# Kernel optimization log

Hardware: AMD Instinct MI355X
Metric: run time of the kernel (lower is better)

## Reference

```python
import jax, jax.numpy as jnp
import numpy as np

MARGIN = 1.0
SAFE_RADIUS = 4.0
B, C, H, W = 16, 48, 64, 64
N_CORR = 2048


def _normalize(x, eps=1e-12):
    # F.normalize(x, dim=0): L2-normalize over the channel axis
    return x / jnp.maximum(jnp.linalg.norm(x, axis=0, keepdims=True), eps)


def _grid_positions(h, w):
    i, j = jnp.meshgrid(jnp.arange(h, dtype=jnp.float32),
                        jnp.arange(w, dtype=jnp.float32), indexing='ij')
    return jnp.stack([i.reshape(-1), j.reshape(-1)], axis=0)


def _per_image(df1, df2, att1, att2, ids, fp2):
    c, h1, w1 = df1.shape
    _, h2, w2 = df2.shape
    all_d1 = _normalize(df1.reshape(c, -1))   # [c, h1*w1]
    all_d2 = _normalize(df2.reshape(c, -1))   # [c, h2*w2]

    d1 = all_d1[:, ids]                       # [c, n] gathered anchors
    s1 = att1.reshape(-1)[ids]                # [n]
    d2 = _normalize(df2[:, fp2[0], fp2[1]])   # [c, n] gathered positives

    positive_distance = 2.0 - 2.0 * jnp.sum(d1 * d2, axis=0)  # [n]

    # hard-negative mining in image 2
    grid2 = _grid_positions(h2, w2)           # [2, h2*w2]
    pd2 = jnp.max(jnp.abs(fp2.astype(jnp.float32)[:, :, None] - grid2[:, None, :]), axis=0)
    out2 = (pd2 > SAFE_RADIUS).astype(df1.dtype)            # [n, h2*w2]
    dm2 = 2.0 - 2.0 * jnp.einsum('cn,cm->nm', d1, all_d2)   # [n, h2*w2]
    neg2 = jnp.min(dm2 + (1.0 - out2) * 10.0, axis=1)       # [n]

    # hard-negative mining in image 1
    grid1 = _grid_positions(h1, w1)
    fp1 = grid1[:, ids]                                      # [2, n]
    pd1 = jnp.max(jnp.abs(fp1[:, :, None] - grid1[:, None, :]), axis=0)
    out1 = (pd1 > SAFE_RADIUS).astype(df1.dtype)
    dm1 = 2.0 - 2.0 * jnp.einsum('cn,cm->nm', d2, all_d1)
    neg1 = jnp.min(dm1 + (1.0 - out1) * 10.0, axis=1)

    diff = positive_distance - jnp.minimum(neg1, neg2)
    s2 = att2[0, fp2[0], fp2[1]]
    w = s1 * s2
    return jnp.sum(w * jax.nn.relu(MARGIN + diff)) / jnp.sum(w)


def setup_inputs() -> dict:
    key = jax.random.key(0)
    k1, k2, k3, k4, k5, k6 = jax.random.split(key, 6)
    return {
        'x1_encoded': jax.random.normal(k1, (B, C, H, W), dtype=jnp.float32),
        'x2_encoded': jax.random.normal(k2, (B, C, H, W), dtype=jnp.float32),
        'attentions1': jax.random.uniform(k3, (B, 1, H, W), dtype=jnp.float32),
        'attentions2': jax.random.uniform(k4, (B, 1, H, W), dtype=jnp.float32),
        'ids': jax.random.randint(k5, (B, N_CORR), 0, H * W),
        'fmap_pos2': jax.random.randint(k6, (B, 2, N_CORR), 0, H),
    }


def reference(x1_encoded, x2_encoded, attentions1, attentions2, ids, fmap_pos2):
    per_image = jax.vmap(_per_image)(x1_encoded, x2_encoded, attentions1,
                                     attentions2, ids, fmap_pos2)
    return jnp.mean(per_image).reshape(1)
```

## Files before the change

### kernel.cpp

```cpp
#include <hip/hip_runtime.h>
#include <stdint.h>

#define BB 16
#define HW 4096
#define NC 2048
#define KHW 72
#define KB 144

typedef __attribute__((ext_vector_type(8))) __bf16 bf16x8;
typedef __attribute__((ext_vector_type(8))) short short8;
typedef __attribute__((ext_vector_type(4))) float floatx4;

static __device__ __forceinline__ unsigned short f2bf(float f) {
    unsigned u = __builtin_bit_cast(unsigned, f);
    unsigned r = u + 0x7fffu + ((u >> 16) & 1u);
    return (unsigned short)(r >> 16);
}

#define GLD16(g, l) __builtin_amdgcn_global_load_lds((const __attribute__((address_space(1))) void*)(g), (__attribute__((address_space(3))) void*)(l), 16, 0, 0)
#define GLD4(g, l)  __builtin_amdgcn_global_load_lds((const __attribute__((address_space(1))) void*)(g), (__attribute__((address_space(3))) void*)(l), 4, 0, 0)

__global__ void prep_fused(const float* __restrict__ x1, const float* __restrict__ x2,
                           const int* __restrict__ ids, const int* __restrict__ fp2,
                           unsigned short* __restrict__ dbp,
                           int* __restrict__ perm, int* __restrict__ qcol_s,
                           int* __restrict__ aqpack, unsigned int* __restrict__ maxs2enc) {
    __shared__ __align__(16) unsigned char slab[36864];
    int bid = blockIdx.x, tid = threadIdx.x;
    if (bid < 512) {
        int img = bid >> 8;
        int b = (bid & 255) >> 4;
        int p0 = (bid & 15) * 256;
        int p = p0 + tid;
        const float* x = img ? x2 : x1;
        const float* col = x + (size_t)b * 48 * HW + p;
        float v[48]; float s = 0.f;
#pragma unroll
        for (int c = 0; c < 48; ++c) { v[c] = col[c * HW]; s = fmaf(v[c], v[c], s); }
        float r = 1.f / fmaxf(sqrtf(s), 1e-12f);
        unsigned short* lcol = (unsigned short*)(slab + tid * KB);
#pragma unroll
        for (int ch = 0; ch < 6; ++ch) {
            union { unsigned u[4]; floatx4 f; } pk;
#pragma unroll
            for (int d = 0; d < 4; ++d) {
                int c = ch * 8 + d * 2;
                pk.u[d] = (unsigned)f2bf(v[c] * r) | ((unsigned)f2bf(v[c + 1] * r) << 16);
            }
            *(floatx4*)(lcol + ch * 8) = pk.f;
        }
        floatx4 z = {0.f, 0.f, 0.f, 0.f};
#pragma unroll
        for (int ch = 6; ch < 9; ++ch) *(floatx4*)(lcol + ch * 8) = z;
        __syncthreads();
        unsigned char* dstb = (unsigned char*)dbp + ((size_t)(img * BB + b) * HW + p0) * KB;
#pragma unroll
        for (int rr = 0; rr < 9; ++rr) {
            int idx = rr * 4096 + tid * 16;
            *(floatx4*)(dstb + idx) = *(const floatx4*)(slab + idx);
        }
    } else if (bid < 544) {
        int* hist = (int*)slab;
        int* base = hist + 64;
        int seg = bid - 512;
        int dir = seg >> 4, b = seg & 15;
        if (tid < 64) hist[tid] = 0;
        __syncthreads();
#pragma unroll
        for (int k = 0; k < 8; ++k) {
            int n = k * 256 + tid;
            int idv = ids[b * NC + n];
            int i2 = fp2[b * 2 * NC + n];
            int qi = (dir == 0) ? i2 : (idv >> 6);
            atomicAdd(&hist[qi], 1);
        }
        __syncthreads();
        if (tid == 0) {
            int run = 0;
            for (int k = 0; k < 64; ++k) { base[k] = run; run += hist[k]; }
        }
        __syncthreads();
#pragma unroll
        for (int k = 0; k < 8; ++k) {
            int n = k * 256 + tid;
            int idv = ids[b * NC + n];
            int i2 = fp2[b * 2 * NC + n];
            int j2 = fp2[b * 2 * NC + NC + n];
            int qi, qj, qcol;
            if (dir == 0) { qi = i2; qj = j2; qcol = idv; }
            else          { qi = idv >> 6; qj = idv & 63; qcol = i2 * 64 + j2; }
            int slot = atomicAdd(&base[qi], 1);
            perm[seg * NC + slot] = n;
            qcol_s[seg * NC + slot] = qcol;
            aqpack[seg * NC + slot] = (qi << 8) | qj;
        }
    } else {
        int t = (bid - 544) * 256 + tid;
        uint4* p = (uint4*)maxs2enc;
        uint4 z = {0u, 0u, 0u, 0u};
#pragma unroll
        for (int k = 0; k < 8; ++k) p[k * 2048 + t] = z;
    }
}

static __device__ __forceinline__ void dma64(const unsigned char* g, unsigned char* l,
                                             int wave, int lane) {
    int wo = wave * 2304;
#pragma unroll
    for (int rr = 0; rr < 2; ++rr)
        GLD16(g + wo + rr * 1024 + lane * 16, l + wo + rr * 1024);
    GLD4(g + wo + 2048 + lane * 4, l + wo + 2048);
}

__global__ __launch_bounds__(256) void maxscore_mfma(
    const unsigned short* __restrict__ dbp,
    const int* __restrict__ perm, const int* __restrict__ qcol_s,
    const int* __restrict__ aqpack, unsigned int* __restrict__ maxs2enc) {
    __shared__ __align__(16) unsigned char smem[18432];

    int tid = threadIdx.x, wave = tid >> 6, lane = tid & 63;
    int quad = lane >> 4, cl = lane & 15;
    int gid = blockIdx.x;
    int seg = gid & 31, dir = seg >> 4, b = seg & 15;
    int rest = gid >> 5, mtile = rest & 7, nq = rest >> 3;
    int qbase = mtile * 256;
    int dbimg = 1 - dir;

    const unsigned char* dbQ = (const unsigned char*)(dbp + (size_t)(dir * BB + b) * HW * KHW);
    short8 afr[4][2];
#pragma unroll
    for (int t = 0; t < 4; ++t) {
        int slot = qbase + wave * 64 + t * 16 + cl;
        int qc = qcol_s[seg * NC + slot];
        const unsigned char* src = dbQ + (size_t)qc * KB;
        afr[t][0] = *(const short8*)(src + quad * 16);
        afr[t][1] = *(const short8*)(src + 64 + quad * 16);
    }
    int aqp2[4][2];
#pragma unroll
    for (int t = 0; t < 4; ++t)
#pragma unroll
        for (int pp = 0; pp < 2; ++pp) {
            int s0 = seg * NC + qbase + wave * 64 + t * 16 + quad * 4 + pp * 2;
            aqp2[t][pp] = aqpack[s0] | (aqpack[s0 + 1] << 16);
        }
    int wb = seg * NC + qbase + wave * 64;
    int qimin = __builtin_amdgcn_readfirstlane(aqpack[wb] >> 8);
    int qimax = __builtin_amdgcn_readfirstlane(aqpack[wb + 63] >> 8);

    const unsigned char* dsrc =
        (const unsigned char*)(dbp + ((size_t)(dbimg * BB + b) * HW + nq * 512) * KHW);
    dma64(dsrc, smem, wave, lane);

    const floatx4 zf = {0.f, 0.f, 0.f, 0.f};
    float cl_f = (float)cl;
    float mx[4][4];
#pragma unroll
    for (int t = 0; t < 4; ++t)
#pragma unroll
        for (int r = 0; r < 4; ++r) mx[t][r] = -1e30f;

    for (int tile = 0; tile < 8; ++tile) {
        unsigned char* buf = smem + (tile & 1) * 9216;
        __syncthreads();
        if (tile + 1 < 8)
            dma64(dsrc + (tile + 1) * 9216, smem + ((tile + 1) & 1) * 9216, wave, lane);
        int mi = nq * 8 + tile;
        bool active = (mi >= qimin - 4) && (mi <= qimax + 4);
        if (active) {
            float mi_f = (float)mi;
            float qjd[4][4];
#pragma unroll
            for (int t = 0; t < 4; ++t)
#pragma unroll
                for (int r = 0; r < 4; ++r) {
                    int ap = (aqp2[t][r >> 1] >> (16 * (r & 1))) & 0xffff;
                    bool rowblk = fabsf((float)(ap >> 8) - mi_f) <= 4.0f;
                    qjd[t][r] = rowblk ? ((float)(ap & 255) - cl_f) : 1e6f;
                }
#pragma unroll
            for (int js = 0; js < 4; ++js) {
                float jj = (float)(js * 16);
                short8 b0 = *(const short8*)(buf + (js * 16 + cl) * KB + quad * 16);
                short8 b1 = *(const short8*)(buf + (js * 16 + cl) * KB + 64 + quad * 16);
#pragma unroll
                for (int t = 0; t < 4; ++t) {
                    floatx4 acc = __builtin_amdgcn_mfma_f32_16x16x32_bf16(
                        __builtin_bit_cast(bf16x8, afr[t][0]),
                        __builtin_bit_cast(bf16x8, b0), zf, 0, 0, 0);
                    acc = __builtin_amdgcn_mfma_f32_16x16x32_bf16(
                        __builtin_bit_cast(bf16x8, afr[t][1]),
                        __builtin_bit_cast(bf16x8, b1), acc, 0, 0, 0);
#pragma unroll
                    for (int r = 0; r < 4; ++r) {
                        bool ok = fabsf(qjd[t][r] - jj) > 4.0f;
                        mx[t][r] = ok ? fmaxf(mx[t][r], acc[r]) : mx[t][r];
                    }
                }
            }
        } else {
#pragma unroll
            for (int js = 0; js < 4; ++js) {
                short8 b0 = *(const short8*)(buf + (js * 16 + cl) * KB + quad * 16);
                short8 b1 = *(const short8*)(buf + (js * 16 + cl) * KB + 64 + quad * 16);
#pragma unroll
                for (int t = 0; t < 4; ++t) {
                    floatx4 acc = __builtin_amdgcn_mfma_f32_16x16x32_bf16(
                        __builtin_bit_cast(bf16x8, afr[t][0]),
                        __builtin_bit_cast(bf16x8, b0), zf, 0, 0, 0);
                    acc = __builtin_amdgcn_mfma_f32_16x16x32_bf16(
                        __builtin_bit_cast(bf16x8, afr[t][1]),
                        __builtin_bit_cast(bf16x8, b1), acc, 0, 0, 0);
#pragma unroll
                    for (int r = 0; r < 4; ++r)
                        mx[t][r] = fmaxf(mx[t][r], acc[r]);
                }
            }
        }
    }

#pragma unroll
    for (int t = 0; t < 4; ++t)
#pragma unroll
        for (int r = 0; r < 4; ++r) {
            float v = mx[t][r];
            v = fmaxf(v, __shfl_xor(v, 1, 16));
            v = fmaxf(v, __shfl_xor(v, 2, 16));
            v = fmaxf(v, __shfl_xor(v, 4, 16));
            v = fmaxf(v, __shfl_xor(v, 8, 16));
            mx[t][r] = v;
        }
    if (cl == 0) {
#pragma unroll
        for (int t = 0; t < 4; ++t)
#pragma unroll
            for (int r = 0; r < 4; ++r) {
                int slot = qbase + wave * 64 + t * 16 + quad * 4 + r;
                int orig = perm[seg * NC + slot];
                float v = mx[t][r] + 2.0f;
                atomicMax(&maxs2enc[(size_t)seg * NC + orig],
                          __builtin_bit_cast(unsigned, v));
            }
    }
}

__global__ void loss_kernel(const float* __restrict__ att1, const float* __restrict__ att2,
                            const int* __restrict__ ids, const int* __restrict__ fp2,
                            const unsigned short* __restrict__ dbp,
                            const unsigned int* __restrict__ maxs2enc,
                            float* __restrict__ pnum, float* __restrict__ pden) {
    int b = blockIdx.x >> 3, chunk = blockIdx.x & 7;
    int tid = threadIdx.x;
    int n = chunk * 256 + tid;
    int idv = ids[b * NC + n];
    int i2 = fp2[b * 2 * NC + n], j2 = fp2[b * 2 * NC + NC + n];
    const uint4* a4 = (const uint4*)(dbp + ((size_t)(0 * BB + b) * HW + idv) * KHW);
    const uint4* b4 = (const uint4*)(dbp + ((size_t)(1 * BB + b) * HW + i2 * 64 + j2) * KHW);
    float dot = 0.f;
#pragma unroll
    for (int i = 0; i < 6; ++i) {
        uint4 xa = a4[i], xb = b4[i];
        const unsigned* xu = (const unsigned*)&xa;
        const unsigned* yu = (const unsigned*)&xb;
#pragma unroll
        for (int w = 0; w < 4; ++w) {
            float xl = __builtin_bit_cast(float, xu[w] << 16);
            float xh = __builtin_bit_cast(float, xu[w] & 0xffff0000u);
            float yl = __builtin_bit_cast(float, yu[w] << 16);
            float yh = __builtin_bit_cast(float, yu[w] & 0xffff0000u);
            dot = fmaf(xl, yl, fmaf(xh, yh, dot));
        }
    }
    float m0 = __builtin_bit_cast(float, maxs2enc[(size_t)(0 * BB + b) * NC + n]) - 2.0f;
    float m1 = __builtin_bit_cast(float, maxs2enc[(size_t)(1 * BB + b) * NC + n]) - 2.0f;
    float ms = fmaxf(m0, m1);
    float diff = (2.f - 2.f * dot) - (2.f - 2.f * ms);
    float w = att1[b * HW + idv] * att2[b * HW + i2 * 64 + j2];
    float num = w * fmaxf(0.f, 1.f + diff);
    float den = w;
    __shared__ float sn[256], sd[256];
    sn[tid] = num; sd[tid] = den;
    __syncthreads();
    for (int s = 128; s > 0; s >>= 1) {
        if (tid < s) { sn[tid] += sn[tid + s]; sd[tid] += sd[tid + s]; }
        __syncthreads();
    }
    if (tid == 0) { pnum[blockIdx.x] = sn[0]; pden[blockIdx.x] = sd[0]; }
}

__global__ void final_kernel(const float* __restrict__ pnum, const float* __restrict__ pden,
                             float* __restrict__ out) {
    int tid = threadIdx.x;
    __shared__ float r[16];
    if (tid < 16) {
        float n = 0.f, d = 0.f;
#pragma unroll
        for (int c = 0; c < 8; ++c) { n += pnum[tid * 8 + c]; d += pden[tid * 8 + c]; }
        r[tid] = n / d;
    }
    __syncthreads();
    if (tid == 0) {
        float s = 0.f;
#pragma unroll
        for (int k = 0; k < 16; ++k) s += r[k];
        out[0] = s * (1.f / BB);
    }
}

extern "C" void kernel_launch(void* const* d_in, const int* in_sizes, int n_in,
                              void* d_out, int out_size, void* d_ws, size_t ws_size,
                              hipStream_t stream) {
    const float* x1  = (const float*)d_in[0];
    const float* x2  = (const float*)d_in[1];
    const float* att1 = (const float*)d_in[2];
    const float* att2 = (const float*)d_in[3];
    const int* ids   = (const int*)d_in[4];
    const int* fp2   = (const int*)d_in[5];
    float* out = (float*)d_out;

    unsigned char* w = (unsigned char*)d_ws;
    unsigned short* dbp = (unsigned short*)(w + 0);
    int* perm    = (int*)(w + 18874368);
    int* qcol_s  = (int*)(w + 19136512);
    int* aqpack  = (int*)(w + 19398656);
    unsigned int* maxs2enc = (unsigned int*)(w + 19660800);
    float* pnum  = (float*)(w + 19922944);
    float* pden  = (float*)(w + 19923456);

    prep_fused<<<dim3(552), dim3(256), 0, stream>>>(x1, x2, ids, fp2, dbp,
                                                    perm, qcol_s, aqpack, maxs2enc);
    maxscore_mfma<<<dim3(2048), dim3(256), 0, stream>>>(dbp, perm, qcol_s, aqpack, maxs2enc);
    loss_kernel<<<dim3(128), dim3(256), 0, stream>>>(att1, att2, ids, fp2, dbp, maxs2enc, pnum, pden);
    final_kernel<<<dim3(1), dim3(64), 0, stream>>>(pnum, pden, out);
}
```

Baseline: 144.5 us.

## Switch max-score kernel to 32x32x16 MFMA with tighter bf16 row padding

The similarity-max kernel moves from 16x16x32 MFMA tiles in 256-thread blocks to single-wave 64-thread blocks using 32x32x16 MFMA. Each block now covers 64 queries and 1024 database columns, double-buffered through LDS with 16-byte global-to-LDS loads. The packed bf16 descriptor row is cut from 144 to 112 bytes (48 channels plus padding), which shrinks both the prep writes and the per-tile DMA. The prep kernel now reads channels with float4 loads per wave and reduces the norms through LDS. The costs are a larger accumulator register footprint and more, smaller blocks, and the loss kernel must read the new 56-element row stride correctly.

After: 174.8 us. 21.0% more time.

```diff
diff --git a/kernel.cpp b/kernel.cpp
--- a/kernel.cpp
+++ b/kernel.cpp
@@ -4,12 +4,13 @@
 #define BB 16
 #define HW 4096
 #define NC 2048
-#define KHW 72
-#define KB 144
+#define KHW 56
+#define KB 112
 
 typedef __attribute__((ext_vector_type(8))) __bf16 bf16x8;
 typedef __attribute__((ext_vector_type(8))) short short8;
 typedef __attribute__((ext_vector_type(4))) float floatx4;
+typedef __attribute__((ext_vector_type(16))) float floatx16;
 
 static __device__ __forceinline__ unsigned short f2bf(float f) {
     unsigned u = __builtin_bit_cast(unsigned, f);
@@ -18,44 +19,54 @@
 }
 
 #define GLD16(g, l) __builtin_amdgcn_global_load_lds((const __attribute__((address_space(1))) void*)(g), (__attribute__((address_space(3))) void*)(l), 16, 0, 0)
-#define GLD4(g, l)  __builtin_amdgcn_global_load_lds((const __attribute__((address_space(1))) void*)(g), (__attribute__((address_space(3))) void*)(l), 4, 0, 0)
 
 __global__ void prep_fused(const float* __restrict__ x1, const float* __restrict__ x2,
                            const int* __restrict__ ids, const int* __restrict__ fp2,
                            unsigned short* __restrict__ dbp,
                            int* __restrict__ perm, int* __restrict__ qcol_s,
                            int* __restrict__ aqpack, unsigned int* __restrict__ maxs2enc) {
-    __shared__ __align__(16) unsigned char slab[36864];
+    __shared__ __align__(16) unsigned char slab[33792];
     int bid = blockIdx.x, tid = threadIdx.x;
     if (bid < 512) {
         int img = bid >> 8;
-        int b = (bid & 255) >> 4;
+        int b = (bid >> 4) & 15;
         int p0 = (bid & 15) * 256;
-        int p = p0 + tid;
+        int w = tid >> 6, l = tid & 63;
         const float* x = img ? x2 : x1;
-        const float* col = x + (size_t)b * 48 * HW + p;
-        float v[48]; float s = 0.f;
-#pragma unroll
-        for (int c = 0; c < 48; ++c) { v[c] = col[c * HW]; s = fmaf(v[c], v[c], s); }
-        float r = 1.f / fmaxf(sqrtf(s), 1e-12f);
-        unsigned short* lcol = (unsigned short*)(slab + tid * KB);
-#pragma unroll
-        for (int ch = 0; ch < 6; ++ch) {
-            union { unsigned u[4]; floatx4 f; } pk;
-#pragma unroll
-            for (int d = 0; d < 4; ++d) {
-                int c = ch * 8 + d * 2;
-                pk.u[d] = (unsigned)f2bf(v[c] * r) | ((unsigned)f2bf(v[c + 1] * r) << 16);
+        const float* base = x + ((size_t)b * 48 + w * 12) * HW + p0 + 4 * l;
+        floatx4 v[12];
+        floatx4 ps = {0.f, 0.f, 0.f, 0.f};
+#pragma unroll
+        for (int cc = 0; cc < 12; ++cc) {
+            v[cc] = *(const floatx4*)(base + cc * HW);
+#pragma unroll
+            for (int q = 0; q < 4; ++q) ps[q] = fmaf(v[cc][q], v[cc][q], ps[q]);
+        }
+        float* psum = (float*)(slab + 28672);
+        float* rbuf = (float*)(slab + 28672 + 4096);
+        *(floatx4*)(psum + w * 256 + 4 * l) = ps;
+        __syncthreads();
+        float s = psum[tid] + psum[256 + tid] + psum[512 + tid] + psum[768 + tid];
+        rbuf[tid] = 1.f / fmaxf(sqrtf(s), 1e-12f);
+        __syncthreads();
+        floatx4 rv = *(const floatx4*)(rbuf + 4 * l);
+#pragma unroll
+        for (int q = 0; q < 4; ++q) {
+            unsigned u[6];
+#pragma unroll
+            for (int p = 0; p < 6; ++p) {
+                u[p] = (unsigned)f2bf(v[2 * p][q] * rv[q]) |
+                       ((unsigned)f2bf(v[2 * p + 1][q] * rv[q]) << 16);
             }
-            *(floatx4*)(lcol + ch * 8) = pk.f;
-        }
-        floatx4 z = {0.f, 0.f, 0.f, 0.f};
-#pragma unroll
-        for (int ch = 6; ch < 9; ++ch) *(floatx4*)(lcol + ch * 8) = z;
+            unsigned char* dst = slab + (4 * l + q) * KB + w * 24;
+            *(uint2*)(dst + 0)  = make_uint2(u[0], u[1]);
+            *(uint2*)(dst + 8)  = make_uint2(u[2], u[3]);
+            *(uint2*)(dst + 16) = make_uint2(u[4], u[5]);
+        }
         __syncthreads();
         unsigned char* dstb = (unsigned char*)dbp + ((size_t)(img * BB + b) * HW + p0) * KB;
 #pragma unroll
-        for (int rr = 0; rr < 9; ++rr) {
+        for (int rr = 0; rr < 7; ++rr) {
             int idx = rr * 4096 + tid * 16;
             *(floatx4*)(dstb + idx) = *(const floatx4*)(slab + idx);
         }
@@ -103,141 +114,143 @@
     }
 }
 
-static __device__ __forceinline__ void dma64(const unsigned char* g, unsigned char* l,
-                                             int wave, int lane) {
-    int wo = wave * 2304;
-#pragma unroll
-    for (int rr = 0; rr < 2; ++rr)
-        GLD16(g + wo + rr * 1024 + lane * 16, l + wo + rr * 1024);
-    GLD4(g + wo + 2048 + lane * 4, l + wo + 2048);
-}
-
-__global__ __launch_bounds__(256) void maxscore_mfma(
+__global__ __launch_bounds__(64) void maxscore_mfma(
     const unsigned short* __restrict__ dbp,
     const int* __restrict__ perm, const int* __restrict__ qcol_s,
     const int* __restrict__ aqpack, unsigned int* __restrict__ maxs2enc) {
-    __shared__ __align__(16) unsigned char smem[18432];
-
-    int tid = threadIdx.x, wave = tid >> 6, lane = tid & 63;
-    int quad = lane >> 4, cl = lane & 15;
+    __shared__ __align__(16) unsigned char smem[14336];
+
+    int lane = threadIdx.x;
+    int ml = lane & 31, hl = lane >> 5;
     int gid = blockIdx.x;
     int seg = gid & 31, dir = seg >> 4, b = seg & 15;
-    int rest = gid >> 5, mtile = rest & 7, nq = rest >> 3;
-    int qbase = mtile * 256;
+    int mtile = (gid >> 5) & 31, nq = gid >> 10;
+    int qbase = mtile * 64;
     int dbimg = 1 - dir;
 
     const unsigned char* dbQ = (const unsigned char*)(dbp + (size_t)(dir * BB + b) * HW * KHW);
-    short8 afr[4][2];
-#pragma unroll
-    for (int t = 0; t < 4; ++t) {
-        int slot = qbase + wave * 64 + t * 16 + cl;
-        int qc = qcol_s[seg * NC + slot];
-        const unsigned char* src = dbQ + (size_t)qc * KB;
-        afr[t][0] = *(const short8*)(src + quad * 16);
-        afr[t][1] = *(const short8*)(src + 64 + quad * 16);
-    }
-    int aqp2[4][2];
-#pragma unroll
-    for (int t = 0; t < 4; ++t)
-#pragma unroll
-        for (int pp = 0; pp < 2; ++pp) {
-            int s0 = seg * NC + qbase + wave * 64 + t * 16 + quad * 4 + pp * 2;
-            aqp2[t][pp] = aqpack[s0] | (aqpack[s0 + 1] << 16);
-        }
-    int wb = seg * NC + qbase + wave * 64;
-    int qimin = __builtin_amdgcn_readfirstlane(aqpack[wb] >> 8);
-    int qimax = __builtin_amdgcn_readfirstlane(aqpack[wb + 63] >> 8);
+    short8 afr[2][3];
+#pragma unroll
+    for (int mc = 0; mc < 2; ++mc) {
+        int qc = qcol_s[seg * NC + qbase + mc * 32 + ml];
+        const unsigned char* src = dbQ + (size_t)qc * KB + hl * 16;
+        afr[mc][0] = *(const short8*)(src);
+        afr[mc][1] = *(const short8*)(src + 32);
+        afr[mc][2] = *(const short8*)(src + 64);
+    }
+    int qp[2][8];
+#pragma unroll
+    for (int mc = 0; mc < 2; ++mc)
+#pragma unroll
+        for (int rp = 0; rp < 8; ++rp) {
+            int rr = 2 * rp;
+            int row = (rr & 3) + 8 * (rr >> 2) + 4 * hl;
+            int slot = seg * NC + qbase + mc * 32 + row;
+            qp[mc][rp] = aqpack[slot] | (aqpack[slot + 1] << 16);
+        }
+    int a0 = aqpack[seg * NC + qbase];
+    int a63 = aqpack[seg * NC + qbase + 63];
+    int qimin = __builtin_amdgcn_readfirstlane(a0 >> 8);
+    int qimax = __builtin_amdgcn_readfirstlane(a63 >> 8);
 
     const unsigned char* dsrc =
-        (const unsigned char*)(dbp + ((size_t)(dbimg * BB + b) * HW + nq * 512) * KHW);
-    dma64(dsrc, smem, wave, lane);
-
-    const floatx4 zf = {0.f, 0.f, 0.f, 0.f};
-    float cl_f = (float)cl;
-    float mx[4][4];
-#pragma unroll
-    for (int t = 0; t < 4; ++t)
-#pragma unroll
-        for (int r = 0; r < 4; ++r) mx[t][r] = -1e30f;
-
-    for (int tile = 0; tile < 8; ++tile) {
-        unsigned char* buf = smem + (tile & 1) * 9216;
-        __syncthreads();
-        if (tile + 1 < 8)
-            dma64(dsrc + (tile + 1) * 9216, smem + ((tile + 1) & 1) * 9216, wave, lane);
-        int mi = nq * 8 + tile;
+        (const unsigned char*)(dbp + ((size_t)(dbimg * BB + b) * HW + nq * 1024) * KHW);
+#pragma unroll
+    for (int rr = 0; rr < 7; ++rr)
+        GLD16(dsrc + rr * 1024 + lane * 16, smem + rr * 1024);
+
+    float mx[2][16];
+#pragma unroll
+    for (int mc = 0; mc < 2; ++mc)
+#pragma unroll
+        for (int rr = 0; rr < 16; ++rr) mx[mc][rr] = -1e30f;
+    float mlf = (float)ml;
+
+    for (int t = 0; t < 16; ++t) {
+        const unsigned char* buf = smem + (t & 1) * 7168;
+        short8 bf[2][3];
+#pragma unroll
+        for (int nc = 0; nc < 2; ++nc)
+#pragma unroll
+            for (int ks = 0; ks < 3; ++ks)
+                bf[nc][ks] = *(const short8*)(buf + (nc * 32 + ml) * KB + ks * 32 + hl * 16);
+        if (t + 1 < 16) {
+            const unsigned char* g = dsrc + (t + 1) * 7168;
+            unsigned char* l = smem + ((t + 1) & 1) * 7168;
+#pragma unroll
+            for (int rr = 0; rr < 7; ++rr)
+                GLD16(g + rr * 1024 + lane * 16, l + rr * 1024);
+        }
+        floatx16 acc[2][2];
+#pragma unroll
+        for (int nc = 0; nc < 2; ++nc)
+#pragma unroll
+            for (int mc = 0; mc < 2; ++mc) {
+                floatx16 a = {};
+                a = __builtin_amdgcn_mfma_f32_32x32x16_bf16(
+                        __builtin_bit_cast(bf16x8, afr[mc][0]),
+                        __builtin_bit_cast(bf16x8, bf[nc][0]), a, 0, 0, 0);
+                a = __builtin_amdgcn_mfma_f32_32x32x16_bf16(
+                        __builtin_bit_cast(bf16x8, afr[mc][1]),
+                        __builtin_bit_cast(bf16x8, bf[nc][1]), a, 0, 0, 0);
+                a = __builtin_amdgcn_mfma_f32_32x32x16_bf16(
+                        __builtin_bit_cast(bf16x8, afr[mc][2]),
+                        __builtin_bit_cast(bf16x8, bf[nc][2]), a, 0, 0, 0);
+                acc[nc][mc] = a;
+            }
+        int mi = nq * 16 + t;
         bool active = (mi >= qimin - 4) && (mi <= qimax + 4);
         if (active) {
             float mi_f = (float)mi;
-            float qjd[4][4];
-#pragma unroll
-            for (int t = 0; t < 4; ++t)
-#pragma unroll
-                for (int r = 0; r < 4; ++r) {
-                    int ap = (aqp2[t][r >> 1] >> (16 * (r & 1))) & 0xffff;
-                    bool rowblk = fabsf((float)(ap >> 8) - mi_f) <= 4.0f;
-                    qjd[t][r] = rowblk ? ((float)(ap & 255) - cl_f) : 1e6f;
-                }
-#pragma unroll
-            for (int js = 0; js < 4; ++js) {
-                float jj = (float)(js * 16);
-                short8 b0 = *(const short8*)(buf + (js * 16 + cl) * KB + quad * 16);
-                short8 b1 = *(const short8*)(buf + (js * 16 + cl) * KB + 64 + quad * 16);
-#pragma unroll
-                for (int t = 0; t < 4; ++t) {
-                    floatx4 acc = __builtin_amdgcn_mfma_f32_16x16x32_bf16(
-                        __builtin_bit_cast(bf16x8, afr[t][0]),
-                        __builtin_bit_cast(bf16x8, b0), zf, 0, 0, 0);
-                    acc = __builtin_amdgcn_mfma_f32_16x16x32_bf16(
-                        __builtin_bit_cast(bf16x8, afr[t][1]),
-                        __builtin_bit_cast(bf16x8, b1), acc, 0, 0, 0);
-#pragma unroll
-                    for (int r = 0; r < 4; ++r) {
-                        bool ok = fabsf(qjd[t][r] - jj) > 4.0f;
-                        mx[t][r] = ok ? fmaxf(mx[t][r], acc[r]) : mx[t][r];
+#pragma unroll
+            for (int mc = 0; mc < 2; ++mc)
+#pragma unroll
+                for (int rp = 0; rp < 8; ++rp) {
+                    int ap2 = qp[mc][rp];
+#pragma unroll
+                    for (int h = 0; h < 2; ++h) {
+                        int rr = 2 * rp + h;
+                        int ap = (ap2 >> (16 * h)) & 0xffff;
+                        bool rowblk = fabsf((float)(ap >> 8) - mi_f) <= 4.0f;
+                        float qjd = rowblk ? (float)(ap & 255) : 1e9f;
+                        float dj0 = qjd - mlf;
+                        float dj1 = qjd - (mlf + 32.0f);
+                        float s0 = (fabsf(dj0) > 4.0f) ? acc[0][mc][rr] : -1e30f;
+                        float s1 = (fabsf(dj1) > 4.0f) ? acc[1][mc][rr] : -1e30f;
+                        mx[mc][rr] = fmaxf(mx[mc][rr], fmaxf(s0, s1));
                     }
                 }
-            }
         } else {
 #pragma unroll
-            for (int js = 0; js < 4; ++js) {
-                short8 b0 = *(const short8*)(buf + (js * 16 + cl) * KB + quad * 16);
-                short8 b1 = *(const short8*)(buf + (js * 16 + cl) * KB + 64 + quad * 16);
-#pragma unroll
-                for (int t = 0; t < 4; ++t) {
-                    floatx4 acc = __builtin_amdgcn_mfma_f32_16x16x32_bf16(
-                        __builtin_bit_cast(bf16x8, afr[t][0]),
-                        __builtin_bit_cast(bf16x8, b0), zf, 0, 0, 0);
-                    acc = __builtin_amdgcn_mfma_f32_16x16x32_bf16(
-                        __builtin_bit_cast(bf16x8, afr[t][1]),
-                        __builtin_bit_cast(bf16x8, b1), acc, 0, 0, 0);
-#pragma unroll
-                    for (int r = 0; r < 4; ++r)
-                        mx[t][r] = fmaxf(mx[t][r], acc[r]);
-                }
-            }
-        }
-    }
-
-#pragma unroll
-    for (int t = 0; t < 4; ++t)
-#pragma unroll
-        for (int r = 0; r < 4; ++r) {
-            float v = mx[t][r];
-            v = fmaxf(v, __shfl_xor(v, 1, 16));
-            v = fmaxf(v, __shfl_xor(v, 2, 16));
-            v = fmaxf(v, __shfl_xor(v, 4, 16));
-            v = fmaxf(v, __shfl_xor(v, 8, 16));
-            mx[t][r] = v;
-        }
-    if (cl == 0) {
-#pragma unroll
-        for (int t = 0; t < 4; ++t)
-#pragma unroll
-            for (int r = 0; r < 4; ++r) {
-                int slot = qbase + wave * 64 + t * 16 + quad * 4 + r;
+            for (int mc = 0; mc < 2; ++mc)
+#pragma unroll
+                for (int rr = 0; rr < 16; ++rr)
+                    mx[mc][rr] = fmaxf(mx[mc][rr],
+                                       fmaxf(acc[0][mc][rr], acc[1][mc][rr]));
+        }
+    }
+
+#pragma unroll
+    for (int mc = 0; mc < 2; ++mc)
+#pragma unroll
+        for (int rr = 0; rr < 16; ++rr) {
+            float v = mx[mc][rr];
+            v = fmaxf(v, __shfl_xor(v, 1, 32));
+            v = fmaxf(v, __shfl_xor(v, 2, 32));
+            v = fmaxf(v, __shfl_xor(v, 4, 32));
+            v = fmaxf(v, __shfl_xor(v, 8, 32));
+            v = fmaxf(v, __shfl_xor(v, 16, 32));
+            mx[mc][rr] = v;
+        }
+    if (ml == 0) {
+#pragma unroll
+        for (int mc = 0; mc < 2; ++mc)
+#pragma unroll
+            for (int rr = 0; rr < 16; ++rr) {
+                int row = (rr & 3) + 8 * (rr >> 2) + 4 * hl;
+                int slot = qbase + mc * 32 + row;
                 int orig = perm[seg * NC + slot];
-                float v = mx[t][r] + 2.0f;
+                float v = mx[mc][rr] + 2.0f;
                 atomicMax(&maxs2enc[(size_t)seg * NC + orig],
                           __builtin_bit_cast(unsigned, v));
             }
@@ -320,16 +333,16 @@
 
     unsigned char* w = (unsigned char*)d_ws;
     unsigned short* dbp = (unsigned short*)(w + 0);
-    int* perm    = (int*)(w + 18874368);
-    int* qcol_s  = (int*)(w + 19136512);
-    int* aqpack  = (int*)(w + 19398656);
-    unsigned int* maxs2enc = (unsigned int*)(w + 19660800);
-    float* pnum  = (float*)(w + 19922944);
-    float* pden  = (float*)(w + 19923456);
+    int* perm    = (int*)(w + 14680064);
+    int* qcol_s  = (int*)(w + 14942208);
+    int* aqpack  = (int*)(w + 15204352);
+    unsigned int* maxs2enc = (unsigned int*)(w + 15466496);
+    float* pnum  = (float*)(w + 15728640);
+    float* pden  = (float*)(w + 15729152);
 
     prep_fused<<<dim3(552), dim3(256), 0, stream>>>(x1, x2, ids, fp2, dbp,
                                                     perm, qcol_s, aqpack, maxs2enc);
-    maxscore_mfma<<<dim3(2048), dim3(256), 0, stream>>>(dbp, perm, qcol_s, aqpack, maxs2enc);
+    maxscore_mfma<<<dim3(4096), dim3(64), 0, stream>>>(dbp, perm, qcol_s, aqpack, maxs2enc);
     loss_kernel<<<dim3(128), dim3(256), 0, stream>>>(att1, att2, ids, fp2, dbp, maxs2enc, pnum, pden);
     final_kernel<<<dim3(1), dim3(64), 0, stream>>>(pnum, pden, out);
 }
```

## Retile MFMA max-score kernel, split by direction, vectorize normalization prep

Applied to the files above, without the earlier changes.

The prep kernel now loads four pixels per thread with 16-byte vector loads across 12-channel slices per wave. It reduces squared norms through shared memory, then writes transposed bf16 rows into the staging slab. The max-score kernel is split into two launches, one per matching direction, and retiled to 128 queries per block (32 per wave) with 1024-column database slabs in double-buffered 18 KB shared tiles. Launch bounds request 4 blocks per SM. This trades less query reuse per wave for lower register pressure and higher occupancy, and adds an extra kernel launch.

After: 136.7 us. 5.4% less time.

```diff
diff --git a/kernel.cpp b/kernel.cpp
--- a/kernel.cpp
+++ b/kernel.cpp
@@ -25,33 +25,48 @@
                            unsigned short* __restrict__ dbp,
                            int* __restrict__ perm, int* __restrict__ qcol_s,
                            int* __restrict__ aqpack, unsigned int* __restrict__ maxs2enc) {
-    __shared__ __align__(16) unsigned char slab[36864];
+    __shared__ __align__(16) unsigned char slab[36864 + 4096 + 1024];
     int bid = blockIdx.x, tid = threadIdx.x;
     if (bid < 512) {
         int img = bid >> 8;
-        int b = (bid & 255) >> 4;
+        int b = (bid >> 4) & 15;
         int p0 = (bid & 15) * 256;
-        int p = p0 + tid;
+        int w = tid >> 6, l = tid & 63;
         const float* x = img ? x2 : x1;
-        const float* col = x + (size_t)b * 48 * HW + p;
-        float v[48]; float s = 0.f;
-#pragma unroll
-        for (int c = 0; c < 48; ++c) { v[c] = col[c * HW]; s = fmaf(v[c], v[c], s); }
-        float r = 1.f / fmaxf(sqrtf(s), 1e-12f);
-        unsigned short* lcol = (unsigned short*)(slab + tid * KB);
-#pragma unroll
-        for (int ch = 0; ch < 6; ++ch) {
-            union { unsigned u[4]; floatx4 f; } pk;
-#pragma unroll
-            for (int d = 0; d < 4; ++d) {
-                int c = ch * 8 + d * 2;
-                pk.u[d] = (unsigned)f2bf(v[c] * r) | ((unsigned)f2bf(v[c + 1] * r) << 16);
+        const float* base = x + ((size_t)b * 48 + w * 12) * HW + p0 + 4 * l;
+        floatx4 v[12];
+        floatx4 ps = {0.f, 0.f, 0.f, 0.f};
+#pragma unroll
+        for (int cc = 0; cc < 12; ++cc) {
+            v[cc] = *(const floatx4*)(base + cc * HW);
+#pragma unroll
+            for (int q = 0; q < 4; ++q) ps[q] = fmaf(v[cc][q], v[cc][q], ps[q]);
+        }
+        float* psum = (float*)(slab + 36864);
+        float* rbuf = (float*)(slab + 36864 + 4096);
+        *(floatx4*)(psum + w * 256 + 4 * l) = ps;
+        __syncthreads();
+        float s = psum[tid] + psum[256 + tid] + psum[512 + tid] + psum[768 + tid];
+        rbuf[tid] = 1.f / fmaxf(sqrtf(s), 1e-12f);
+        __syncthreads();
+        floatx4 rv = *(const floatx4*)(rbuf + 4 * l);
+#pragma unroll
+        for (int q = 0; q < 4; ++q) {
+            unsigned u[6];
+#pragma unroll
+            for (int p = 0; p < 6; ++p) {
+                u[p] = (unsigned)f2bf(v[2 * p][q] * rv[q]) |
+                       ((unsigned)f2bf(v[2 * p + 1][q] * rv[q]) << 16);
             }
-            *(floatx4*)(lcol + ch * 8) = pk.f;
-        }
-        floatx4 z = {0.f, 0.f, 0.f, 0.f};
-#pragma unroll
-        for (int ch = 6; ch < 9; ++ch) *(floatx4*)(lcol + ch * 8) = z;
+            unsigned char* dst = slab + (4 * l + q) * KB + w * 24;
+            *(uint2*)(dst + 0)  = make_uint2(u[0], u[1]);
+            *(uint2*)(dst + 8)  = make_uint2(u[2], u[3]);
+            *(uint2*)(dst + 16) = make_uint2(u[4], u[5]);
+        }
+        uint4 z4 = {0u, 0u, 0u, 0u};
+#pragma unroll
+        for (int z = 0; z < 3; ++z)
+            *(uint4*)(slab + tid * KB + 96 + z * 16) = z4;
         __syncthreads();
         unsigned char* dstb = (unsigned char*)dbp + ((size_t)(img * BB + b) * HW + p0) * KB;
 #pragma unroll
@@ -103,124 +118,134 @@
     }
 }
 
-static __device__ __forceinline__ void dma64(const unsigned char* g, unsigned char* l,
-                                             int wave, int lane) {
-    int wo = wave * 2304;
+static __device__ __forceinline__ void dma_tile(const unsigned char* g, unsigned char* l,
+                                                int wave, int lane) {
+#pragma unroll
+    for (int rr = 0; rr < 4; ++rr)
+        GLD16(g + rr * 4096 + wave * 1024 + lane * 16, l + rr * 4096 + wave * 1024);
 #pragma unroll
     for (int rr = 0; rr < 2; ++rr)
-        GLD16(g + wo + rr * 1024 + lane * 16, l + wo + rr * 1024);
-    GLD4(g + wo + 2048 + lane * 4, l + wo + 2048);
-}
-
-__global__ __launch_bounds__(256) void maxscore_mfma(
+        GLD4(g + 16384 + rr * 1024 + wave * 256 + lane * 4, l + 16384 + rr * 1024 + wave * 256);
+}
+
+template <int DIR>
+__device__ __forceinline__ void maxscore_core(
     const unsigned short* __restrict__ dbp,
     const int* __restrict__ perm, const int* __restrict__ qcol_s,
     const int* __restrict__ aqpack, unsigned int* __restrict__ maxs2enc) {
-    __shared__ __align__(16) unsigned char smem[18432];
+    __shared__ __align__(16) unsigned char smem[36864];
 
     int tid = threadIdx.x, wave = tid >> 6, lane = tid & 63;
     int quad = lane >> 4, cl = lane & 15;
     int gid = blockIdx.x;
-    int seg = gid & 31, dir = seg >> 4, b = seg & 15;
-    int rest = gid >> 5, mtile = rest & 7, nq = rest >> 3;
-    int qbase = mtile * 256;
-    int dbimg = 1 - dir;
-
-    const unsigned char* dbQ = (const unsigned char*)(dbp + (size_t)(dir * BB + b) * HW * KHW);
-    short8 afr[4][2];
-#pragma unroll
-    for (int t = 0; t < 4; ++t) {
-        int slot = qbase + wave * 64 + t * 16 + cl;
+    int b = gid & 15;
+    int mtile = (gid >> 4) & 15, nq = gid >> 8;
+    int seg = DIR * BB + b;
+    int qbase = mtile * 128;
+    int dbimg = 1 - DIR;
+
+    const unsigned char* dbQ = (const unsigned char*)(dbp + (size_t)(DIR * BB + b) * HW * KHW);
+    short8 afr[2][2];
+#pragma unroll
+    for (int t = 0; t < 2; ++t) {
+        int slot = qbase + wave * 32 + t * 16 + cl;
         int qc = qcol_s[seg * NC + slot];
         const unsigned char* src = dbQ + (size_t)qc * KB;
         afr[t][0] = *(const short8*)(src + quad * 16);
         afr[t][1] = *(const short8*)(src + 64 + quad * 16);
     }
-    int aqp2[4][2];
-#pragma unroll
-    for (int t = 0; t < 4; ++t)
-#pragma unroll
-        for (int pp = 0; pp < 2; ++pp) {
-            int s0 = seg * NC + qbase + wave * 64 + t * 16 + quad * 4 + pp * 2;
-            aqp2[t][pp] = aqpack[s0] | (aqpack[s0 + 1] << 16);
-        }
-    int wb = seg * NC + qbase + wave * 64;
+    float qif[2][4], qjc[2][4];
+    float cl_f = (float)cl;
+#pragma unroll
+    for (int t = 0; t < 2; ++t)
+#pragma unroll
+        for (int r = 0; r < 4; ++r) {
+            int slot = qbase + wave * 32 + t * 16 + quad * 4 + r;
+            int ap = aqpack[seg * NC + slot];
+            qif[t][r] = (float)(ap >> 8);
+            qjc[t][r] = (float)(ap & 255) - cl_f;
+        }
+    int wb = seg * NC + qbase + wave * 32;
     int qimin = __builtin_amdgcn_readfirstlane(aqpack[wb] >> 8);
-    int qimax = __builtin_amdgcn_readfirstlane(aqpack[wb + 63] >> 8);
+    int qimax = __builtin_amdgcn_readfirstlane(aqpack[wb + 31] >> 8);
 
     const unsigned char* dsrc =
-        (const unsigned char*)(dbp + ((size_t)(dbimg * BB + b) * HW + nq * 512) * KHW);
-    dma64(dsrc, smem, wave, lane);
+        (const unsigned char*)(dbp + ((size_t)(dbimg * BB + b) * HW + nq * 1024) * KHW);
+    dma_tile(dsrc, smem, wave, lane);
 
     const floatx4 zf = {0.f, 0.f, 0.f, 0.f};
-    float cl_f = (float)cl;
-    float mx[4][4];
-#pragma unroll
-    for (int t = 0; t < 4; ++t)
+    float mx[2][4];
+#pragma unroll
+    for (int t = 0; t < 2; ++t)
 #pragma unroll
         for (int r = 0; r < 4; ++r) mx[t][r] = -1e30f;
 
     for (int tile = 0; tile < 8; ++tile) {
-        unsigned char* buf = smem + (tile & 1) * 9216;
+        unsigned char* buf = smem + (tile & 1) * 18432;
         __syncthreads();
         if (tile + 1 < 8)
-            dma64(dsrc + (tile + 1) * 9216, smem + ((tile + 1) & 1) * 9216, wave, lane);
-        int mi = nq * 8 + tile;
-        bool active = (mi >= qimin - 4) && (mi <= qimax + 4);
-        if (active) {
-            float mi_f = (float)mi;
-            float qjd[4][4];
-#pragma unroll
-            for (int t = 0; t < 4; ++t)
-#pragma unroll
-                for (int r = 0; r < 4; ++r) {
-                    int ap = (aqp2[t][r >> 1] >> (16 * (r & 1))) & 0xffff;
-                    bool rowblk = fabsf((float)(ap >> 8) - mi_f) <= 4.0f;
-                    qjd[t][r] = rowblk ? ((float)(ap & 255) - cl_f) : 1e6f;
+            dma_tile(dsrc + (tile + 1) * 18432, smem + ((tile + 1) & 1) * 18432, wave, lane);
+        int mi0 = (nq * 1024 + tile * 128) >> 6;
+#pragma unroll
+        for (int half = 0; half < 2; ++half) {
+            int mi = mi0 + half;
+            bool active = (mi >= qimin - 4) && (mi <= qimax + 4);
+            if (active) {
+                float mi_f = (float)mi;
+                float qjd[2][4];
+#pragma unroll
+                for (int t = 0; t < 2; ++t)
+#pragma unroll
+                    for (int r = 0; r < 4; ++r) {
+                        bool rowblk = fabsf(qif[t][r] - mi_f) <= 4.0f;
+                        qjd[t][r] = rowblk ? qjc[t][r] : 1e9f;
+                    }
+#pragma unroll
+                for (int js = 0; js < 4; ++js) {
+                    int sub = half * 4 + js;
+                    float jj = (float)(js * 16);
+                    short8 b0 = *(const short8*)(buf + (sub * 16 + cl) * KB + quad * 16);
+                    short8 b1 = *(const short8*)(buf + (sub * 16 + cl) * KB + 64 + quad * 16);
+#pragma unroll
+                    for (int t = 0; t < 2; ++t) {
+                        floatx4 acc = __builtin_amdgcn_mfma_f32_16x16x32_bf16(
+                            __builtin_bit_cast(bf16x8, afr[t][0]),
+                            __builtin_bit_cast(bf16x8, b0), zf, 0, 0, 0);
+                        acc = __builtin_amdgcn_mfma_f32_16x16x32_bf16(
+                            __builtin_bit_cast(bf16x8, afr[t][1]),
+                            __builtin_bit_cast(bf16x8, b1), acc, 0, 0, 0);
+#pragma unroll
+                        for (int r = 0; r < 4; ++r) {
+                            bool ok = fabsf(qjd[t][r] - jj) > 4.0f;
+                            mx[t][r] = ok ? fmaxf(mx[t][r], acc[r]) : mx[t][r];
+                        }
+                    }
                 }
-#pragma unroll
-            for (int js = 0; js < 4; ++js) {
-                float jj = (float)(js * 16);
-                short8 b0 = *(const short8*)(buf + (js * 16 + cl) * KB + quad * 16);
-                short8 b1 = *(const short8*)(buf + (js * 16 + cl) * KB + 64 + quad * 16);
-#pragma unroll
-                for (int t = 0; t < 4; ++t) {
-                    floatx4 acc = __builtin_amdgcn_mfma_f32_16x16x32_bf16(
-                        __builtin_bit_cast(bf16x8, afr[t][0]),
-                        __builtin_bit_cast(bf16x8, b0), zf, 0, 0, 0);
-                    acc = __builtin_amdgcn_mfma_f32_16x16x32_bf16(
-                        __builtin_bit_cast(bf16x8, afr[t][1]),
-                        __builtin_bit_cast(bf16x8, b1), acc, 0, 0, 0);
-#pragma unroll
-                    for (int r = 0; r < 4; ++r) {
-                        bool ok = fabsf(qjd[t][r] - jj) > 4.0f;
-                        mx[t][r] = ok ? fmaxf(mx[t][r], acc[r]) : mx[t][r];
+            } else {
+#pragma unroll
+                for (int js = 0; js < 4; ++js) {
+                    int sub = half * 4 + js;
+                    short8 b0 = *(const short8*)(buf + (sub * 16 + cl) * KB + quad * 16);
+                    short8 b1 = *(const short8*)(buf + (sub * 16 + cl) * KB + 64 + quad * 16);
+#pragma unroll
+                    for (int t = 0; t < 2; ++t) {
+                        floatx4 acc = __builtin_amdgcn_mfma_f32_16x16x32_bf16(
+                            __builtin_bit_cast(bf16x8, afr[t][0]),
+                            __builtin_bit_cast(bf16x8, b0), zf, 0, 0, 0);
+                        acc = __builtin_amdgcn_mfma_f32_16x16x32_bf16(
+                            __builtin_bit_cast(bf16x8, afr[t][1]),
+                            __builtin_bit_cast(bf16x8, b1), acc, 0, 0, 0);
+#pragma unroll
+                        for (int r = 0; r < 4; ++r)
+                            mx[t][r] = fmaxf(mx[t][r], acc[r]);
                     }
                 }
             }
-        } else {
-#pragma unroll
-            for (int js = 0; js < 4; ++js) {
-                short8 b0 = *(const short8*)(buf + (js * 16 + cl) * KB + quad * 16);
-                short8 b1 = *(const short8*)(buf + (js * 16 + cl) * KB + 64 + quad * 16);
-#pragma unroll
-                for (int t = 0; t < 4; ++t) {
-                    floatx4 acc = __builtin_amdgcn_mfma_f32_16x16x32_bf16(
-                        __builtin_bit_cast(bf16x8, afr[t][0]),
-                        __builtin_bit_cast(bf16x8, b0), zf, 0, 0, 0);
-                    acc = __builtin_amdgcn_mfma_f32_16x16x32_bf16(
-                        __builtin_bit_cast(bf16x8, afr[t][1]),
-                        __builtin_bit_cast(bf16x8, b1), acc, 0, 0, 0);
-#pragma unroll
-                    for (int r = 0; r < 4; ++r)
-                        mx[t][r] = fmaxf(mx[t][r], acc[r]);
-                }
-            }
-        }
-    }
-
-#pragma unroll
-    for (int t = 0; t < 4; ++t)
+        }
+    }
+
+#pragma unroll
+    for (int t = 0; t < 2; ++t)
 #pragma unroll
         for (int r = 0; r < 4; ++r) {
             float v = mx[t][r];
@@ -232,16 +257,29 @@
         }
     if (cl == 0) {
 #pragma unroll
-        for (int t = 0; t < 4; ++t)
+        for (int t = 0; t < 2; ++t)
 #pragma unroll
             for (int r = 0; r < 4; ++r) {
-                int slot = qbase + wave * 64 + t * 16 + quad * 4 + r;
+                int slot = qbase + wave * 32 + t * 16 + quad * 4 + r;
                 int orig = perm[seg * NC + slot];
                 float v = mx[t][r] + 2.0f;
                 atomicMax(&maxs2enc[(size_t)seg * NC + orig],
                           __builtin_bit_cast(unsigned, v));
             }
     }
+}
+
+__global__ __launch_bounds__(256, 4) void maxscore_d0(
+    const unsigned short* __restrict__ dbp, const int* __restrict__ perm,
+    const int* __restrict__ qcol_s, const int* __restrict__ aqpack,
+    unsigned int* __restrict__ maxs2enc) {
+    maxscore_core<0>(dbp, perm, qcol_s, aqpack, maxs2enc);
+}
+__global__ __launch_bounds__(256, 4) void maxscore_d1(
+    const unsigned short* __restrict__ dbp, const int* __restrict__ perm,
+    const int* __restrict__ qcol_s, const int* __restrict__ aqpack,
+    unsigned int* __restrict__ maxs2enc) {
+    maxscore_core<1>(dbp, perm, qcol_s, aqpack, maxs2enc);
 }
 
 __global__ void loss_kernel(const float* __restrict__ att1, const float* __restrict__ att2,
@@ -329,7 +367,8 @@
 
     prep_fused<<<dim3(552), dim3(256), 0, stream>>>(x1, x2, ids, fp2, dbp,
                                                     perm, qcol_s, aqpack, maxs2enc);
-    maxscore_mfma<<<dim3(2048), dim3(256), 0, stream>>>(dbp, perm, qcol_s, aqpack, maxs2enc);
+    maxscore_d0<<<dim3(1024), dim3(256), 0, stream>>>(dbp, perm, qcol_s, aqpack, maxs2enc);
+    maxscore_d1<<<dim3(1024), dim3(256), 0, stream>>>(dbp, perm, qcol_s, aqpack, maxs2enc);
     loss_kernel<<<dim3(128), dim3(256), 0, stream>>>(att1, att2, ids, fp2, dbp, maxs2enc, pnum, pden);
     final_kernel<<<dim3(1), dim3(64), 0, stream>>>(pnum, pden, out);
 }
```
